# Performance work log

Hardware: AMD Instinct MI355X
Metric: run time of the kernel (lower is better)

Reference implementation:

```python
import jax, jax.numpy as jnp
import numpy as np

EPS = 1e-6


def _mp_cos_pointwise(p, q, M2):
    # p, q: [B, L, K]; M2: [C, K] (squared perspective weights)
    # cosine between (p*M_c) and (q*M_c) along K, per channel c -> [B, L, C]
    num = jnp.einsum('blk,blk,ck->blc', p, q, M2)
    pn = jnp.sqrt(jnp.maximum(jnp.einsum('blk,ck->blc', p * p, M2), EPS))
    qn = jnp.sqrt(jnp.maximum(jnp.einsum('blk,ck->blc', q * q, M2), EPS))
    return num / pn / qn


def setup_inputs() -> dict:
    key = jax.random.key(0)
    ks = jax.random.split(key, 10)
    B, Lq, Ld, K, C = 32, 200, 200, 200, 50
    f32 = jnp.float32
    def unif(k, shape):  # keras 'uniform' init: U(-0.05, 0.05)
        return jax.random.uniform(k, shape, f32, -0.05, 0.05)
    return {
        'q_rep': jax.random.normal(ks[0], (B, Lq, K), f32),
        'q_last': jax.random.normal(ks[1], (B, K), f32),
        'q_mask': jnp.ones((B, Lq), f32),
        'd_rep': jax.random.normal(ks[2], (B, Ld, K), f32),
        'd_last': jax.random.normal(ks[3], (B, K), f32),
        'd_mask': jnp.ones((B, Ld), f32),
        'full_M': unif(ks[4], (C, K)),
        'maxpool_M': unif(ks[5], (C, K)),
        'att_M': unif(ks[6], (C, K)),
        'max_att_M': unif(ks[7], (C, K)),
    }


def reference(q_rep, q_last, q_mask, d_rep, d_last, d_mask,
              full_M, maxpool_M, att_M, max_att_M):
    outputs = []

    # relevancy matrix: cosine(q[b,j,:], d[b,i,:]) -> [B, Ld, Lq]
    num = jnp.einsum('bik,bjk->bij', d_rep, q_rep)
    dn = jnp.sqrt(jnp.maximum(jnp.sum(d_rep * d_rep, -1), EPS))  # [B, Ld]
    qn = jnp.sqrt(jnp.maximum(jnp.sum(q_rep * q_rep, -1), EPS))  # [B, Lq]
    rel = num / qn[:, None, :] / dn[:, :, None]
    rel = rel * q_mask[:, None, :] * d_mask[:, :, None]

    # full matching: cosine(d[b,i]*M_c, q_last[b]*M_c) -> [B, Ld, C]
    M2 = full_M * full_M
    fnum = jnp.einsum('bik,bk,ck->bic', d_rep, q_last, M2)
    fpn = jnp.sqrt(jnp.maximum(jnp.einsum('bik,ck->bic', d_rep * d_rep, M2), EPS))
    fqn = jnp.sqrt(jnp.maximum(jnp.einsum('bk,ck->bc', q_last * q_last, M2), EPS))
    outputs.append(fnum / fpn / fqn[:, None, :])

    # maxpool matching: cosine(d[b,i]*M_c, q[b,j]*M_c) -> [B, Ld, Lq, C]
    M2 = maxpool_M * maxpool_M
    mnum = jnp.einsum('bik,bjk,ck->bijc', d_rep, q_rep, M2)
    mpn = jnp.sqrt(jnp.maximum(jnp.einsum('bik,ck->bic', d_rep * d_rep, M2), EPS))
    mqn = jnp.sqrt(jnp.maximum(jnp.einsum('bjk,ck->bjc', q_rep * q_rep, M2), EPS))
    mm = mnum / mpn[:, :, None, :] / mqn[:, None, :, :]
    outputs.append(jnp.concatenate([jnp.max(mm, axis=2), jnp.mean(mm, axis=2)], axis=2))

    # attentive matching: cosine-weighted q rep (no softmax -> normalize by sum)
    wq = jnp.einsum('bij,bjk->bik', rel, q_rep)
    wq = wq / (jnp.sum(rel, axis=-1) + EPS)[..., None]  # [B, Ld, K]
    outputs.append(_mp_cos_pointwise(d_rep, wq, att_M * att_M))

    # max-attentive matching: gather best-matching q word per d position
    idx = jnp.argmax(rel, axis=2)  # [B, Ld]
    max_q = jnp.take_along_axis(q_rep, idx[:, :, None], axis=1)  # [B, Ld, K]
    outputs.append(_mp_cos_pointwise(d_rep, max_q, max_att_M * max_att_M))

    return jnp.concatenate(outputs, axis=-1)  # [B, Ld, 5*C]
```

## Files before the change

kernel.cpp:

```cpp
#include <hip/hip_runtime.h>
#include <math.h>


#define EPS 1e-6f
#define NEG_HUGE -3.4e38f

typedef __bf16 bf16x8 __attribute__((ext_vector_type(8)));
typedef float f32x16 __attribute__((ext_vector_type(16)));

constexpr size_t OFF_M2ALL = 0;
constexpr size_t OFF_M2B16 = 40000;
constexpr size_t OFF_QB16  = 63296;
constexpr size_t OFF_DB16  = 915264;
constexpr size_t OFF_INVFPN= 1767232;
constexpr size_t OFF_INVMPN= 2087232;
constexpr size_t OFF_INVAPN= 2407232;
constexpr size_t OFF_INVXPN= 2727232;
constexpr size_t OFF_INVMQN= 3047232;
constexpr size_t OFF_INVXQN= 3367232;
constexpr size_t OFF_INVFQN= 3687232;
constexpr size_t OFF_INVDN = 3688832;
constexpr size_t OFF_INVQN = 3695232;
constexpr size_t OFF_IDX   = 3701632;
constexpr size_t OFF_WQ    = 3708032;
constexpr size_t OFF_G     = 4988032;
constexpr size_t OFF_PMAX2 = 6268032;
constexpr size_t OFF_PSUM2 = 6677632;

__global__ __launch_bounds__(256) void k_prep(
    const float* __restrict__ qR, const float* __restrict__ dR,
    const float* __restrict__ fM, const float* __restrict__ mM,
    const float* __restrict__ aM, const float* __restrict__ xM,
    unsigned short* __restrict__ qb16, unsigned short* __restrict__ db16,
    float* __restrict__ invdn, float* __restrict__ invqn,
    float* __restrict__ m2all, unsigned short* __restrict__ m2b16)
{
  int blk = blockIdx.x;
  int tid = threadIdx.x;
  if (blk < 4096) {
    int task = blk*4 + (tid >> 6);
    int l = tid & 63;
    int isQ = task >= 8192;
    int r = isQ ? task - 8192 : task;
    int b = r >> 8, j = r & 255;
    unsigned short* dst = (isQ ? qb16 : db16) + (size_t)r*208;
    if (j < 200) {
      const float* src = (isQ ? qR : dR) + (size_t)(b*200 + j)*200;
      float4 v = {0.f,0.f,0.f,0.f};
      if (l < 50) v = *(const float4*)(src + l*4);
      float s = fmaf(v.x,v.x, fmaf(v.y,v.y, fmaf(v.z,v.z, v.w*v.w)));
#pragma unroll
      for (int m = 32; m; m >>= 1) s += __shfl_xor(s, m);
      if (l == 0) {
        float rr = rsqrtf(fmaxf(s, EPS));
        if (isQ) invqn[b*200 + j] = rr; else invdn[b*200 + j] = rr;
      }
      if (l < 52) {
        ushort4 o = {0,0,0,0};
        if (l < 50) {
          __bf16 h0=(__bf16)v.x, h1=(__bf16)v.y, h2=(__bf16)v.z, h3=(__bf16)v.w;
          o.x = *(unsigned short*)&h0; o.y = *(unsigned short*)&h1;
          o.z = *(unsigned short*)&h2; o.w = *(unsigned short*)&h3;
        }
        *(ushort4*)(dst + l*4) = o;
      }
    } else {
      if (l < 52) { ushort4 z = {0,0,0,0}; *(ushort4*)(dst + l*4) = z; }
    }
  } else {
    int i = (blk - 4096)*256 + tid;
    if (i < 40000) {
      int m = i / 10000, r = i % 10000;
      const float* s = (m==0)?fM:(m==1)?mM:(m==2)?aM:xM;
      float v = s[r];
      m2all[i] = v*v;
    }
    if (i < 224*208) {
      int row = i / 208, k = i % 208;
      unsigned short o = 0;
      if (row < 200 && k < 200) {
        int m = row / 50, c = row % 50;
        const float* s = (m==0)?fM:(m==1)?mM:(m==2)?aM:xM;
        float v = s[c*200 + k];
        __bf16 h = (__bf16)(v*v);
        o = *(unsigned short*)&h;
      }
      m2b16[i] = o;
    }
  }
}

__global__ __launch_bounds__(256) void k_mid(
    const float* __restrict__ dR, const float* __restrict__ qR,
    const float* __restrict__ qL, const unsigned short* __restrict__ m2b16,
    float* __restrict__ invfpn, float* __restrict__ invmpn,
    float* __restrict__ invapn, float* __restrict__ invxpn,
    float* __restrict__ invmqn, float* __restrict__ invxqn,
    float* __restrict__ invfqn,
    const float* __restrict__ qMask, const float* __restrict__ dMask,
    const float* __restrict__ invdn, const float* __restrict__ invqn,
    float* __restrict__ wq, int* __restrict__ idxout)
{
  int tid = threadIdx.x;
  if (blockIdx.x < 702) {
    int w = tid >> 6, lane = tid & 63;
    int n = lane & 31, h = lane >> 5;
    int task = blockIdx.x*4 + w;
    if (task >= 2807) return;
    int rt = task / 7, nt = task % 7;
    int row = rt*32 + n;

    const float* src;
    if (row < 6400)       src = dR + (size_t)row*200;
    else if (row < 12800) src = qR + (size_t)(row-6400)*200;
    else                  src = qL + (size_t)(row-12800)*200;

    bf16x8 afrag[13];
#pragma unroll
    for (int ks = 0; ks < 13; ks++) {
      int ko = ks*16 + h*8;
      bf16x8 af;
      if (ko < 200) {
        float4 a0 = *(const float4*)(src + ko);
        float4 a1 = *(const float4*)(src + ko + 4);
        af[0] = (__bf16)(a0.x*a0.x); af[1] = (__bf16)(a0.y*a0.y);
        af[2] = (__bf16)(a0.z*a0.z); af[3] = (__bf16)(a0.w*a0.w);
        af[4] = (__bf16)(a1.x*a1.x); af[5] = (__bf16)(a1.y*a1.y);
        af[6] = (__bf16)(a1.z*a1.z); af[7] = (__bf16)(a1.w*a1.w);
      } else {
#pragma unroll
        for (int z = 0; z < 8; z++) af[z] = (__bf16)0.0f;
      }
      afrag[ks] = af;
    }

    f32x16 C;
#pragma unroll
    for (int z = 0; z < 16; z++) C[z] = 0.f;
    const unsigned short* bp = m2b16 + (size_t)(nt*32 + n)*208 + h*8;
#pragma unroll
    for (int ks = 0; ks < 13; ks++) {
      bf16x8 bf = *(const bf16x8*)(bp + ks*16);
      C = __builtin_amdgcn_mfma_f32_32x32x16_bf16(afrag[ks], bf, C, 0, 0, 0);
    }

    int cp = nt*32 + n;
    if (cp < 200) {
      int m = cp / 50, c = cp % 50;
#pragma unroll
      for (int r = 0; r < 16; r++) {
        int grow = rt*32 + (r & 3) + 8*(r >> 2) + 4*h;
        float v = rsqrtf(fmaxf(C[r], EPS));
        if (grow < 6400) {
          if (m == 0)      invfpn[grow*50 + c] = v;
          else if (m == 1) invmpn[grow*50 + c] = v;
          else if (m == 2) invapn[grow*50 + c] = v;
          else             invxpn[grow*50 + c] = v;
        } else if (grow < 12800) {
          int r2 = grow - 6400;
          if (m == 1)      invmqn[c*6400 + r2] = v;
          else if (m == 3) invxqn[r2*50 + c] = v;
        } else {
          if (m == 0)      invfqn[(grow-12800)*50 + c] = v;
        }
      }
    }
  } else {
    __shared__ float relsh[8][256];
    __shared__ float redv[4][8][2];
    __shared__ int   redi[4][8];
    __shared__ float invrs_sh[8];
    int blk = blockIdx.x - 702;
    int b  = blk / 25;
    int i0 = (blk % 25) * 8;
    int j = tid, jr = min(j, 199);
    bool jv = j < 200;
    const float* qb = qR + b*40000;
    const float* db = dR + (b*200 + i0)*200;
    float acc[8];
#pragma unroll
    for (int ii = 0; ii < 8; ii++) acc[ii] = 0.f;

    const float* qrow = qb + jr*200;
    for (int k4 = 0; k4 < 200; k4 += 4) {
      float4 qv = *(const float4*)(qrow + k4);
#pragma unroll
      for (int ii = 0; ii < 8; ii++) {
        acc[ii] = fmaf(db[ii*200 + k4 + 0], qv.x, acc[ii]);
        acc[ii] = fmaf(db[ii*200 + k4 + 1], qv.y, acc[ii]);
        acc[ii] = fmaf(db[ii*200 + k4 + 2], qv.z, acc[ii]);
        acc[ii] = fmaf(db[ii*200 + k4 + 3], qv.w, acc[ii]);
      }
    }

    float iqn = invqn[b*200 + jr];
    float qm  = qMask[b*200 + jr];
    int w = tid >> 6, l = tid & 63;
    float rv[8];
#pragma unroll
    for (int ii = 0; ii < 8; ii++) {
      float idn = invdn[b*200 + i0 + ii];
      float dm  = dMask[b*200 + i0 + ii];
      float r = acc[ii]*iqn*idn*qm*dm;
      rv[ii] = r;
      relsh[ii][j] = jv ? r : 0.f;
    }
#pragma unroll
    for (int ii = 0; ii < 8; ii++) {
      float vm = jv ? rv[ii] : NEG_HUGE;
      float vs = jv ? rv[ii] : 0.f;
      int bj = jr;
#pragma unroll
      for (int m = 32; m; m >>= 1) {
        float ov = __shfl_xor(vm, m);
        int   oj = __shfl_xor(bj, m);
        vs += __shfl_xor(vs, m);
        if (ov > vm || (ov == vm && oj < bj)) { vm = ov; bj = oj; }
      }
      if (l == 0) { redv[w][ii][0] = vm; redv[w][ii][1] = vs; redi[w][ii] = bj; }
    }
    __syncthreads();
    if (tid < 8) {
      float bv = redv[0][tid][0], ss = redv[0][tid][1]; int bj = redi[0][tid];
      for (int w2 = 1; w2 < 4; w2++) {
        ss += redv[w2][tid][1];
        float wv = redv[w2][tid][0]; int wj = redi[w2][tid];
        if (wv > bv || (wv == bv && wj < bj)) { bv = wv; bj = wj; }
      }
      invrs_sh[tid] = 1.f/(ss + EPS);
      idxout[b*200 + i0 + tid] = bj;
    }
    __syncthreads();

    int kl = min(tid, 199); bool kv = tid < 200;
    float acw[8];
#pragma unroll
    for (int ii = 0; ii < 8; ii++) acw[ii] = 0.f;
    for (int j0 = 0; j0 < 200; j0 += 4) {
      float qv0 = qb[(j0+0)*200 + kl];
      float qv1 = qb[(j0+1)*200 + kl];
      float qv2 = qb[(j0+2)*200 + kl];
      float qv3 = qb[(j0+3)*200 + kl];
#pragma unroll
      for (int ii = 0; ii < 8; ii++) {
        float4 rs = *(const float4*)&relsh[ii][j0];
        acw[ii] = fmaf(rs.x, qv0, acw[ii]);
        acw[ii] = fmaf(rs.y, qv1, acw[ii]);
        acw[ii] = fmaf(rs.z, qv2, acw[ii]);
        acw[ii] = fmaf(rs.w, qv3, acw[ii]);
      }
    }
#pragma unroll
    for (int ii = 0; ii < 8; ii++) {
      float v = acw[ii]*invrs_sh[ii];
      if (kv) wq[(size_t)(b*200 + i0 + ii)*200 + tid] = v;
    }
  }
}

__global__ __launch_bounds__(512,2) void k_big(
    const unsigned short* __restrict__ db16, const unsigned short* __restrict__ qb16,
    const float* __restrict__ m2all, const float* __restrict__ invmqn,
    float* __restrict__ pmax2, float* __restrict__ psum2,
    const float* __restrict__ dR, const float* __restrict__ qR,
    const float* __restrict__ qL, const float* __restrict__ wq,
    const int* __restrict__ idx, const unsigned short* __restrict__ m2b16,
    float* __restrict__ G)
{
  int tid = threadIdx.x;
  int w = tid >> 6, lane = tid & 63;
  int n = lane & 31, h = lane >> 5;
  if (blockIdx.x < 1600) {
    __shared__ __align__(16) unsigned short qsh[128*216];
    int b = blockIdx.x / 50, c = blockIdx.x % 50;
    const float* M2 = m2all + 10000 + c*200;
    const unsigned short* dbp = db16 + (size_t)(b*256 + w*32 + n)*208 + h*8;

    bf16x8 afrag[13];
#pragma unroll
    for (int ks = 0; ks < 13; ks++) afrag[ks] = *(const bf16x8*)(dbp + ks*16);

    float vm[16], vs[16];
#pragma unroll
    for (int r = 0; r < 16; r++) { vm[r] = NEG_HUGE; vs[r] = 0.f; }

    for (int jh = 0; jh < 2; jh++) {
      int nrows = jh ? 96 : 128;
      int njt   = jh ? 3 : 4;
      __syncthreads();
      {
        const unsigned short* src = qb16 + (size_t)(b*256 + jh*128)*208;
        const float* iqb = invmqn + c*6400 + b*200;
        for (int s = tid; s < nrows*26; s += 512) {
          int r = s / 26, ch = s - r*26;
          int j = jh*128 + r;
          float iq = (j < 200) ? iqb[j] : 0.f;
          int k0 = ch*8;
          bf16x8 v = *(const bf16x8*)(src + (size_t)r*208 + k0);
          float4 m0 = *(const float4*)(M2 + k0);
          float4 m1 = *(const float4*)(M2 + k0 + 4);
          bf16x8 o;
          o[0] = (__bf16)((float)v[0]*iq*m0.x); o[1] = (__bf16)((float)v[1]*iq*m0.y);
          o[2] = (__bf16)((float)v[2]*iq*m0.z); o[3] = (__bf16)((float)v[3]*iq*m0.w);
          o[4] = (__bf16)((float)v[4]*iq*m1.x); o[5] = (__bf16)((float)v[5]*iq*m1.y);
          o[6] = (__bf16)((float)v[6]*iq*m1.z); o[7] = (__bf16)((float)v[7]*iq*m1.w);
          *(bf16x8*)(qsh + r*216 + k0) = o;
        }
      }
      __syncthreads();

      for (int jt = 0; jt < njt; jt++) {
        f32x16 C;
#pragma unroll
        for (int z = 0; z < 16; z++) C[z] = 0.f;
        const unsigned short* bptr = qsh + (jt*32 + n)*216 + h*8;
#pragma unroll
        for (int ks = 0; ks < 13; ks++) {
          bf16x8 bf = *(const bf16x8*)(bptr + ks*16);
          C = __builtin_amdgcn_mfma_f32_32x32x16_bf16(afrag[ks], bf, C, 0, 0, 0);
        }
        bool jv = (jh*128 + jt*32 + n) < 200;
#pragma unroll
        for (int r = 0; r < 16; r++) {
          vm[r] = fmaxf(vm[r], jv ? C[r] : NEG_HUGE);
          vs[r] += C[r];
        }
      }
    }

#pragma unroll
    for (int r = 0; r < 16; r++) {
      float a = vm[r], s = vs[r];
#pragma unroll
      for (int m = 1; m <= 16; m <<= 1) {
        a = fmaxf(a, __shfl_xor(a, m));
        s += __shfl_xor(s, m);
      }
      vm[r] = a; vs[r] = s;
    }
    if (n == 0) {
#pragma unroll
      for (int r = 0; r < 16; r++) {
        int i = w*32 + (r & 3) + 8*(r >> 2) + 4*h;
        pmax2[(size_t)blockIdx.x*256 + i] = vm[r];
        psum2[(size_t)blockIdx.x*256 + i] = vs[r];
      }
    }
  } else {
    int task = (blockIdx.x - 1600)*8 + w;
    int mp = task / 400;
    int sub = task % 400;
    int rt = sub >> 1, nt = sub & 1;
    int row = rt*32 + n;
    int bb = row / 200;
    int msel = (mp == 0) ? 0 : (mp == 3) ? 3 : 2;

    const float* s0 = dR + (size_t)row*200;
    const float* s1;
    if (mp == 0)      s1 = qL + (size_t)bb*200;
    else if (mp == 1) s1 = wq + (size_t)row*200;
    else if (mp == 2) { s0 = wq + (size_t)row*200; s1 = s0; }
    else              s1 = qR + (size_t)(bb*200 + idx[row])*200;

    bf16x8 afrag[13];
#pragma unroll
    for (int ks = 0; ks < 13; ks++) {
      int ko = ks*16 + h*8;
      bf16x8 af;
      if (ko < 200) {
        float4 a0 = *(const float4*)(s0 + ko);
        float4 a1 = *(const float4*)(s0 + ko + 4);
        float4 b0 = *(const float4*)(s1 + ko);
        float4 b1 = *(const float4*)(s1 + ko + 4);
        af[0] = (__bf16)(a0.x*b0.x); af[1] = (__bf16)(a0.y*b0.y);
        af[2] = (__bf16)(a0.z*b0.z); af[3] = (__bf16)(a0.w*b0.w);
        af[4] = (__bf16)(a1.x*b1.x); af[5] = (__bf16)(a1.y*b1.y);
        af[6] = (__bf16)(a1.z*b1.z); af[7] = (__bf16)(a1.w*b1.w);
      } else {
#pragma unroll
        for (int z = 0; z < 8; z++) af[z] = (__bf16)0.0f;
      }
      afrag[ks] = af;
    }

    f32x16 C;
#pragma unroll
    for (int z = 0; z < 16; z++) C[z] = 0.f;
    const unsigned short* bp = m2b16 + (size_t)(msel*50 + nt*32 + n)*208 + h*8;
#pragma unroll
    for (int ks = 0; ks < 13; ks++) {
      bf16x8 bf = *(const bf16x8*)(bp + ks*16);
      C = __builtin_amdgcn_mfma_f32_32x32x16_bf16(afrag[ks], bf, C, 0, 0, 0);
    }
    int cc = nt*32 + n;
    if (cc < 50) {
#pragma unroll
      for (int r = 0; r < 16; r++) {
        int mrow = (r & 3) + 8*(r >> 2) + 4*h;
        G[(size_t)(mp*6400 + rt*32 + mrow)*50 + cc] = C[r];
      }
    }
  }
}

__global__ void k_out(
    const float* __restrict__ G, const float* __restrict__ pmax2,
    const float* __restrict__ psum2, const float* __restrict__ invfpn,
    const float* __restrict__ invmpn, const float* __restrict__ invapn,
    const float* __restrict__ invxpn, const float* __restrict__ invfqn,
    const float* __restrict__ invxqn, const int* __restrict__ idx,
    float* __restrict__ out)
{
  int row = blockIdx.x;
  int l = threadIdx.x;
  if (l >= 250) return;
  int b = row / 200, i = row % 200;
  int seg = l / 50, c = l % 50;
  float o;
  if (seg == 0) {
    o = G[(size_t)(0*6400 + row)*50 + c] * invfpn[row*50 + c] * invfqn[b*50 + c];
  } else if (seg == 1) {
    o = pmax2[(size_t)(b*50 + c)*256 + i] * invmpn[row*50 + c];
  } else if (seg == 2) {
    o = psum2[(size_t)(b*50 + c)*256 + i] * invmpn[row*50 + c] * (1.f/200.f);
  } else if (seg == 3) {
    o = G[(size_t)(1*6400 + row)*50 + c] * invapn[row*50 + c]
        * rsqrtf(fmaxf(G[(size_t)(2*6400 + row)*50 + c], EPS));
  } else {
    int jid = idx[row];
    o = G[(size_t)(3*6400 + row)*50 + c] * invxpn[row*50 + c]
        * invxqn[(b*200 + jid)*50 + c];
  }
  out[(size_t)row*250 + l] = o;
}

extern "C" void kernel_launch(void* const* d_in, const int* in_sizes, int n_in,
                              void* d_out, int out_size, void* d_ws, size_t ws_size,
                              hipStream_t stream) {
  const float* qR = (const float*)d_in[0];
  const float* qL = (const float*)d_in[1];
  const float* qM = (const float*)d_in[2];
  const float* dR = (const float*)d_in[3];
  const float* dM = (const float*)d_in[5];
  const float* fullM = (const float*)d_in[6];
  const float* mpM   = (const float*)d_in[7];
  const float* attM  = (const float*)d_in[8];
  const float* xM    = (const float*)d_in[9];

  float* ws  = (float*)d_ws;
  float* out = (float*)d_out;

  float* m2all  = ws + OFF_M2ALL;
  unsigned short* m2b16 = (unsigned short*)(ws + OFF_M2B16);
  unsigned short* qb16 = (unsigned short*)(ws + OFF_QB16);
  unsigned short* db16 = (unsigned short*)(ws + OFF_DB16);
  float* invfpn = ws + OFF_INVFPN;
  float* invmpn = ws + OFF_INVMPN;
  float* invapn = ws + OFF_INVAPN;
  float* invxpn = ws + OFF_INVXPN;
  float* invmqn = ws + OFF_INVMQN;
  float* invxqn = ws + OFF_INVXQN;
  float* invfqn = ws + OFF_INVFQN;
  float* invdn  = ws + OFF_INVDN;
  float* invqn  = ws + OFF_INVQN;
  int*   idxp   = (int*)(ws + OFF_IDX);
  float* wqp    = ws + OFF_WQ;
  float* G      = ws + OFF_G;
  float* pmax2  = ws + OFF_PMAX2;
  float* psum2  = ws + OFF_PSUM2;

  k_prep<<<4278, 256, 0, stream>>>(qR, dR, fullM, mpM, attM, xM,
                                   qb16, db16, invdn, invqn, m2all, m2b16);
  k_mid<<<1502, 256, 0, stream>>>(dR, qR, qL, m2b16,
                                  invfpn, invmpn, invapn, invxpn,
                                  invmqn, invxqn, invfqn,
                                  qM, dM, invdn, invqn, wqp, idxp);
  k_big<<<1800, 512, 0, stream>>>(db16, qb16, m2all, invmqn, pmax2, psum2,
                                  dR, qR, qL, wqp, idxp, m2b16, G);
  k_out<<<6400, 256, 0, stream>>>(G, pmax2, psum2, invfpn, invmpn, invapn,
                                  invxpn, invfqn, invxqn, idxp, out);
}
```

Measured before the change: 248.1 us.

## Fuse four kernels into two and fold normalizations into maxpool operands

Collapses the prep, mid, big and out kernels into a main kernel and a final kernel. The main kernel runs the maxpool MFMA, the relevancy/attention path and the norm GEMMs as separate block ranges. The maxpool path pre-scales q rows by the inverse norm and the squared weights when staging them into shared memory, so the max/mean reduction needs no division afterwards. The final kernel computes the full, attentive and max-attentive GEMMs and writes the output directly, dropping the intermediate G buffer and the bf16 staging copies. This removes launches and global round trips, at the cost of recomputing row norms inside blocks and a heavier single kernel with a large shared-memory union.

```diff
diff --git a/kernel.cpp b/kernel.cpp
--- a/kernel.cpp
+++ b/kernel.cpp
@@ -8,179 +8,194 @@
 typedef __bf16 bf16x8 __attribute__((ext_vector_type(8)));
 typedef float f32x16 __attribute__((ext_vector_type(16)));
 
-constexpr size_t OFF_M2ALL = 0;
-constexpr size_t OFF_M2B16 = 40000;
-constexpr size_t OFF_QB16  = 63296;
-constexpr size_t OFF_DB16  = 915264;
-constexpr size_t OFF_INVFPN= 1767232;
-constexpr size_t OFF_INVMPN= 2087232;
-constexpr size_t OFF_INVAPN= 2407232;
-constexpr size_t OFF_INVXPN= 2727232;
-constexpr size_t OFF_INVMQN= 3047232;
-constexpr size_t OFF_INVXQN= 3367232;
-constexpr size_t OFF_INVFQN= 3687232;
-constexpr size_t OFF_INVDN = 3688832;
-constexpr size_t OFF_INVQN = 3695232;
-constexpr size_t OFF_IDX   = 3701632;
-constexpr size_t OFF_WQ    = 3708032;
-constexpr size_t OFF_G     = 4988032;
-constexpr size_t OFF_PMAX2 = 6268032;
-constexpr size_t OFF_PSUM2 = 6677632;
-
-__global__ __launch_bounds__(256) void k_prep(
+constexpr size_t OFF_INVFPN = 0;
+constexpr size_t OFF_INVMPN = 320000;
+constexpr size_t OFF_INVAPN = 640000;
+constexpr size_t OFF_INVXPN = 960000;
+constexpr size_t OFF_INVMQN = 1280000;
+constexpr size_t OFF_INVXQN = 1600000;
+constexpr size_t OFF_INVFQN = 1920000;
+constexpr size_t OFF_IDX    = 1921600;
+constexpr size_t OFF_WQ     = 1928000;
+constexpr size_t OFF_PMAX2  = 3208000;
+constexpr size_t OFF_PSUM2  = 3617600;
+
+struct MPShared {
+  unsigned short qsh[128*216];
+  float m2sh[208];
+  float iqsh[200];
+};
+struct RWShared {
+  float relsh[2][8][256];
+  float iqn[2][200];
+  float idn[2][8];
+  float redv[2][4][8][2];
+  int   redi[2][4][8];
+  float invrs[2][8];
+};
+union KShared { MPShared mp; RWShared rw; };
+
+__global__ __launch_bounds__(512,2) void k_main(
     const float* __restrict__ qR, const float* __restrict__ dR,
+    const float* __restrict__ qL,
+    const float* __restrict__ qMask, const float* __restrict__ dMask,
     const float* __restrict__ fM, const float* __restrict__ mM,
     const float* __restrict__ aM, const float* __restrict__ xM,
-    unsigned short* __restrict__ qb16, unsigned short* __restrict__ db16,
-    float* __restrict__ invdn, float* __restrict__ invqn,
-    float* __restrict__ m2all, unsigned short* __restrict__ m2b16)
-{
-  int blk = blockIdx.x;
-  int tid = threadIdx.x;
-  if (blk < 4096) {
-    int task = blk*4 + (tid >> 6);
-    int l = tid & 63;
-    int isQ = task >= 8192;
-    int r = isQ ? task - 8192 : task;
-    int b = r >> 8, j = r & 255;
-    unsigned short* dst = (isQ ? qb16 : db16) + (size_t)r*208;
-    if (j < 200) {
-      const float* src = (isQ ? qR : dR) + (size_t)(b*200 + j)*200;
-      float4 v = {0.f,0.f,0.f,0.f};
-      if (l < 50) v = *(const float4*)(src + l*4);
-      float s = fmaf(v.x,v.x, fmaf(v.y,v.y, fmaf(v.z,v.z, v.w*v.w)));
-#pragma unroll
-      for (int m = 32; m; m >>= 1) s += __shfl_xor(s, m);
-      if (l == 0) {
-        float rr = rsqrtf(fmaxf(s, EPS));
-        if (isQ) invqn[b*200 + j] = rr; else invdn[b*200 + j] = rr;
-      }
-      if (l < 52) {
-        ushort4 o = {0,0,0,0};
-        if (l < 50) {
-          __bf16 h0=(__bf16)v.x, h1=(__bf16)v.y, h2=(__bf16)v.z, h3=(__bf16)v.w;
-          o.x = *(unsigned short*)&h0; o.y = *(unsigned short*)&h1;
-          o.z = *(unsigned short*)&h2; o.w = *(unsigned short*)&h3;
-        }
-        *(ushort4*)(dst + l*4) = o;
-      }
-    } else {
-      if (l < 52) { ushort4 z = {0,0,0,0}; *(ushort4*)(dst + l*4) = z; }
-    }
-  } else {
-    int i = (blk - 4096)*256 + tid;
-    if (i < 40000) {
-      int m = i / 10000, r = i % 10000;
-      const float* s = (m==0)?fM:(m==1)?mM:(m==2)?aM:xM;
-      float v = s[r];
-      m2all[i] = v*v;
-    }
-    if (i < 224*208) {
-      int row = i / 208, k = i % 208;
-      unsigned short o = 0;
-      if (row < 200 && k < 200) {
-        int m = row / 50, c = row % 50;
-        const float* s = (m==0)?fM:(m==1)?mM:(m==2)?aM:xM;
-        float v = s[c*200 + k];
-        __bf16 h = (__bf16)(v*v);
-        o = *(unsigned short*)&h;
-      }
-      m2b16[i] = o;
-    }
-  }
-}
-
-__global__ __launch_bounds__(256) void k_mid(
-    const float* __restrict__ dR, const float* __restrict__ qR,
-    const float* __restrict__ qL, const unsigned short* __restrict__ m2b16,
     float* __restrict__ invfpn, float* __restrict__ invmpn,
     float* __restrict__ invapn, float* __restrict__ invxpn,
     float* __restrict__ invmqn, float* __restrict__ invxqn,
     float* __restrict__ invfqn,
-    const float* __restrict__ qMask, const float* __restrict__ dMask,
-    const float* __restrict__ invdn, const float* __restrict__ invqn,
-    float* __restrict__ wq, int* __restrict__ idxout)
+    float* __restrict__ wq, int* __restrict__ idxout,
+    float* __restrict__ pmax2, float* __restrict__ psum2)
 {
+  __shared__ KShared sh;
   int tid = threadIdx.x;
-  if (blockIdx.x < 702) {
-    int w = tid >> 6, lane = tid & 63;
-    int n = lane & 31, h = lane >> 5;
-    int task = blockIdx.x*4 + w;
-    if (task >= 2807) return;
-    int rt = task / 7, nt = task % 7;
-    int row = rt*32 + n;
-
-    const float* src;
-    if (row < 6400)       src = dR + (size_t)row*200;
-    else if (row < 12800) src = qR + (size_t)(row-6400)*200;
-    else                  src = qL + (size_t)(row-12800)*200;
-
+  int blk = blockIdx.x;
+  int w = tid >> 6, lane = tid & 63;
+  int n = lane & 31, h = lane >> 5;
+
+  if (blk < 1600) {
+    int b = blk / 50, c = blk % 50;
+    if (tid < 52) {
+      int k = tid*4;
+      float4 o = {0.f,0.f,0.f,0.f};
+      if (k < 200) {
+        float4 v = *(const float4*)(mM + c*200 + k);
+        o.x=v.x*v.x; o.y=v.y*v.y; o.z=v.z*v.z; o.w=v.w*v.w;
+      }
+      *(float4*)(sh.mp.m2sh + k) = o;
+    }
+    __syncthreads();
+    {
+      const float* qb = qR + b*40000;
+      for (int j = w*25; j < w*25 + 25; j++) {
+        const float* qr = qb + j*200;
+        float s = 0.f;
+        for (int k = lane; k < 200; k += 64) { float v = qr[k]; s = fmaf(v*v, sh.mp.m2sh[k], s); }
+#pragma unroll
+        for (int m = 32; m; m >>= 1) s += __shfl_xor(s, m);
+        if (lane == 0) sh.mp.iqsh[j] = rsqrtf(fmaxf(s, EPS));
+      }
+    }
     bf16x8 afrag[13];
-#pragma unroll
-    for (int ks = 0; ks < 13; ks++) {
-      int ko = ks*16 + h*8;
-      bf16x8 af;
-      if (ko < 200) {
-        float4 a0 = *(const float4*)(src + ko);
-        float4 a1 = *(const float4*)(src + ko + 4);
-        af[0] = (__bf16)(a0.x*a0.x); af[1] = (__bf16)(a0.y*a0.y);
-        af[2] = (__bf16)(a0.z*a0.z); af[3] = (__bf16)(a0.w*a0.w);
-        af[4] = (__bf16)(a1.x*a1.x); af[5] = (__bf16)(a1.y*a1.y);
-        af[6] = (__bf16)(a1.z*a1.z); af[7] = (__bf16)(a1.w*a1.w);
-      } else {
-#pragma unroll
-        for (int z = 0; z < 8; z++) af[z] = (__bf16)0.0f;
-      }
-      afrag[ks] = af;
-    }
-
-    f32x16 C;
-#pragma unroll
-    for (int z = 0; z < 16; z++) C[z] = 0.f;
-    const unsigned short* bp = m2b16 + (size_t)(nt*32 + n)*208 + h*8;
-#pragma unroll
-    for (int ks = 0; ks < 13; ks++) {
-      bf16x8 bf = *(const bf16x8*)(bp + ks*16);
-      C = __builtin_amdgcn_mfma_f32_32x32x16_bf16(afrag[ks], bf, C, 0, 0, 0);
-    }
-
-    int cp = nt*32 + n;
-    if (cp < 200) {
-      int m = cp / 50, c = cp % 50;
+    {
+      int i = w*32 + n, ir = min(i, 199);
+      const float* drow = dR + (size_t)(b*200 + ir)*200;
+#pragma unroll
+      for (int ks = 0; ks < 13; ks++) {
+        int ko = ks*16 + h*8;
+        bf16x8 af;
+        if (ko < 200) {
+          float4 a0 = *(const float4*)(drow + ko);
+          float4 a1 = *(const float4*)(drow + ko + 4);
+          af[0]=(__bf16)a0.x; af[1]=(__bf16)a0.y; af[2]=(__bf16)a0.z; af[3]=(__bf16)a0.w;
+          af[4]=(__bf16)a1.x; af[5]=(__bf16)a1.y; af[6]=(__bf16)a1.z; af[7]=(__bf16)a1.w;
+        } else {
+#pragma unroll
+          for (int z = 0; z < 8; z++) af[z] = (__bf16)0.0f;
+        }
+        afrag[ks] = af;
+      }
+    }
+    float vm[16], vs[16];
+#pragma unroll
+    for (int r = 0; r < 16; r++) { vm[r] = NEG_HUGE; vs[r] = 0.f; }
+
+    for (int jh = 0; jh < 2; jh++) {
+      int nrows = jh ? 96 : 128;
+      int njt   = jh ? 3 : 4;
+      __syncthreads();
+      {
+        const float* qb = qR + b*40000;
+        for (int s = tid; s < nrows*26; s += 512) {
+          int r = s / 26, ch = s - r*26;
+          int j = jh*128 + r;
+          int k0 = ch*8;
+          bf16x8 o;
+          if (j < 200 && k0 < 200) {
+            const float* qr = qb + (size_t)j*200 + k0;
+            float4 v0 = *(const float4*)qr;
+            float4 v1 = *(const float4*)(qr + 4);
+            float iq = sh.mp.iqsh[j];
+            o[0]=(__bf16)(v0.x*iq*sh.mp.m2sh[k0+0]); o[1]=(__bf16)(v0.y*iq*sh.mp.m2sh[k0+1]);
+            o[2]=(__bf16)(v0.z*iq*sh.mp.m2sh[k0+2]); o[3]=(__bf16)(v0.w*iq*sh.mp.m2sh[k0+3]);
+            o[4]=(__bf16)(v1.x*iq*sh.mp.m2sh[k0+4]); o[5]=(__bf16)(v1.y*iq*sh.mp.m2sh[k0+5]);
+            o[6]=(__bf16)(v1.z*iq*sh.mp.m2sh[k0+6]); o[7]=(__bf16)(v1.w*iq*sh.mp.m2sh[k0+7]);
+          } else {
+#pragma unroll
+            for (int z = 0; z < 8; z++) o[z] = (__bf16)0.0f;
+          }
+          *(bf16x8*)(sh.mp.qsh + r*216 + k0) = o;
+        }
+      }
+      __syncthreads();
+      for (int jt = 0; jt < njt; jt++) {
+        f32x16 C;
+#pragma unroll
+        for (int z = 0; z < 16; z++) C[z] = 0.f;
+        const unsigned short* bptr = sh.mp.qsh + (jt*32 + n)*216 + h*8;
+#pragma unroll
+        for (int ks = 0; ks < 13; ks++) {
+          bf16x8 bf = *(const bf16x8*)(bptr + ks*16);
+          C = __builtin_amdgcn_mfma_f32_32x32x16_bf16(afrag[ks], bf, C, 0, 0, 0);
+        }
+        bool jv = (jh*128 + jt*32 + n) < 200;
+#pragma unroll
+        for (int r = 0; r < 16; r++) {
+          vm[r] = fmaxf(vm[r], jv ? C[r] : NEG_HUGE);
+          vs[r] += C[r];
+        }
+      }
+    }
+#pragma unroll
+    for (int r = 0; r < 16; r++) {
+      float a = vm[r], s = vs[r];
+#pragma unroll
+      for (int m = 1; m <= 16; m <<= 1) { a = fmaxf(a, __shfl_xor(a, m)); s += __shfl_xor(s, m); }
+      vm[r] = a; vs[r] = s;
+    }
+    if (n == 0) {
 #pragma unroll
       for (int r = 0; r < 16; r++) {
-        int grow = rt*32 + (r & 3) + 8*(r >> 2) + 4*h;
-        float v = rsqrtf(fmaxf(C[r], EPS));
-        if (grow < 6400) {
-          if (m == 0)      invfpn[grow*50 + c] = v;
-          else if (m == 1) invmpn[grow*50 + c] = v;
-          else if (m == 2) invapn[grow*50 + c] = v;
-          else             invxpn[grow*50 + c] = v;
-        } else if (grow < 12800) {
-          int r2 = grow - 6400;
-          if (m == 1)      invmqn[c*6400 + r2] = v;
-          else if (m == 3) invxqn[r2*50 + c] = v;
-        } else {
-          if (m == 0)      invfqn[(grow-12800)*50 + c] = v;
-        }
-      }
-    }
-  } else {
-    __shared__ float relsh[8][256];
-    __shared__ float redv[4][8][2];
-    __shared__ int   redi[4][8];
-    __shared__ float invrs_sh[8];
-    int blk = blockIdx.x - 702;
-    int b  = blk / 25;
-    int i0 = (blk % 25) * 8;
-    int j = tid, jr = min(j, 199);
+        int i = w*32 + (r & 3) + 8*(r >> 2) + 4*h;
+        pmax2[(size_t)blk*256 + i] = vm[r];
+        psum2[(size_t)blk*256 + i] = vs[r];
+      }
+    }
+  } else if (blk < 2000) {
+    int u = tid >> 8;
+    int tid2 = tid & 255;
+    int unit = (blk - 1600)*2 + u;
+    int b = unit / 25, i0 = (unit % 25)*8;
+    int w2 = tid2 >> 6, l = lane;
+    int j = tid2, jr = min(j, 199);
     bool jv = j < 200;
     const float* qb = qR + b*40000;
     const float* db = dR + (b*200 + i0)*200;
+
+    for (int jq = w2*50; jq < w2*50 + 50; jq++) {
+      float4 v = {0.f,0.f,0.f,0.f};
+      if (l < 50) v = *(const float4*)(qb + jq*200 + l*4);
+      float s = fmaf(v.x,v.x, fmaf(v.y,v.y, fmaf(v.z,v.z, v.w*v.w)));
+#pragma unroll
+      for (int m = 32; m; m >>= 1) s += __shfl_xor(s, m);
+      if (l == 0) sh.rw.iqn[u][jq] = rsqrtf(fmaxf(s, EPS));
+    }
+    if (w2 == 0) {
+      for (int ii = 0; ii < 8; ii++) {
+        float4 v = {0.f,0.f,0.f,0.f};
+        if (l < 50) v = *(const float4*)(db + ii*200 + l*4);
+        float s = fmaf(v.x,v.x, fmaf(v.y,v.y, fmaf(v.z,v.z, v.w*v.w)));
+#pragma unroll
+        for (int m = 32; m; m >>= 1) s += __shfl_xor(s, m);
+        if (l == 0) sh.rw.idn[u][ii] = rsqrtf(fmaxf(s, EPS));
+      }
+    }
+    __syncthreads();
+
     float acc[8];
 #pragma unroll
     for (int ii = 0; ii < 8; ii++) acc[ii] = 0.f;
-
     const float* qrow = qb + jr*200;
     for (int k4 = 0; k4 < 200; k4 += 4) {
       float4 qv = *(const float4*)(qrow + k4);
@@ -192,47 +207,45 @@
         acc[ii] = fmaf(db[ii*200 + k4 + 3], qv.w, acc[ii]);
       }
     }
-
-    float iqn = invqn[b*200 + jr];
+    float iqnv = sh.rw.iqn[u][jr];
     float qm  = qMask[b*200 + jr];
-    int w = tid >> 6, l = tid & 63;
     float rv[8];
 #pragma unroll
     for (int ii = 0; ii < 8; ii++) {
-      float idn = invdn[b*200 + i0 + ii];
-      float dm  = dMask[b*200 + i0 + ii];
-      float r = acc[ii]*iqn*idn*qm*dm;
+      float idnv = sh.rw.idn[u][ii];
+      float dm = dMask[b*200 + i0 + ii];
+      float r = acc[ii]*iqnv*idnv*qm*dm;
       rv[ii] = r;
-      relsh[ii][j] = jv ? r : 0.f;
+      sh.rw.relsh[u][ii][j] = jv ? r : 0.f;
     }
 #pragma unroll
     for (int ii = 0; ii < 8; ii++) {
-      float vm = jv ? rv[ii] : NEG_HUGE;
-      float vs = jv ? rv[ii] : 0.f;
+      float vmv = jv ? rv[ii] : NEG_HUGE;
+      float vsv = jv ? rv[ii] : 0.f;
       int bj = jr;
 #pragma unroll
       for (int m = 32; m; m >>= 1) {
-        float ov = __shfl_xor(vm, m);
+        float ov = __shfl_xor(vmv, m);
         int   oj = __shfl_xor(bj, m);
-        vs += __shfl_xor(vs, m);
-        if (ov > vm || (ov == vm && oj < bj)) { vm = ov; bj = oj; }
-      }
-      if (l == 0) { redv[w][ii][0] = vm; redv[w][ii][1] = vs; redi[w][ii] = bj; }
+        vsv += __shfl_xor(vsv, m);
+        if (ov > vmv || (ov == vmv && oj < bj)) { vmv = ov; bj = oj; }
+      }
+      if (l == 0) { sh.rw.redv[u][w2][ii][0] = vmv; sh.rw.redv[u][w2][ii][1] = vsv; sh.rw.redi[u][w2][ii] = bj; }
     }
     __syncthreads();
-    if (tid < 8) {
-      float bv = redv[0][tid][0], ss = redv[0][tid][1]; int bj = redi[0][tid];
-      for (int w2 = 1; w2 < 4; w2++) {
-        ss += redv[w2][tid][1];
-        float wv = redv[w2][tid][0]; int wj = redi[w2][tid];
+    if (tid2 < 8) {
+      float bv = sh.rw.redv[u][0][tid2][0], ss = sh.rw.redv[u][0][tid2][1];
+      int bj = sh.rw.redi[u][0][tid2];
+      for (int w3 = 1; w3 < 4; w3++) {
+        ss += sh.rw.redv[u][w3][tid2][1];
+        float wv = sh.rw.redv[u][w3][tid2][0]; int wj = sh.rw.redi[u][w3][tid2];
         if (wv > bv || (wv == bv && wj < bj)) { bv = wv; bj = wj; }
       }
-      invrs_sh[tid] = 1.f/(ss + EPS);
-      idxout[b*200 + i0 + tid] = bj;
+      sh.rw.invrs[u][tid2] = 1.f/(ss + EPS);
+      idxout[b*200 + i0 + tid2] = bj;
     }
     __syncthreads();
-
-    int kl = min(tid, 199); bool kv = tid < 200;
+    int kl = min(tid2, 199); bool kv = tid2 < 200;
     float acw[8];
 #pragma unroll
     for (int ii = 0; ii < 8; ii++) acw[ii] = 0.f;
@@ -243,7 +256,7 @@
       float qv3 = qb[(j0+3)*200 + kl];
 #pragma unroll
       for (int ii = 0; ii < 8; ii++) {
-        float4 rs = *(const float4*)&relsh[ii][j0];
+        float4 rs = *(const float4*)&sh.rw.relsh[u][ii][j0];
         acw[ii] = fmaf(rs.x, qv0, acw[ii]);
         acw[ii] = fmaf(rs.y, qv1, acw[ii]);
         acw[ii] = fmaf(rs.z, qv2, acw[ii]);
@@ -252,186 +265,208 @@
     }
 #pragma unroll
     for (int ii = 0; ii < 8; ii++) {
-      float v = acw[ii]*invrs_sh[ii];
-      if (kv) wq[(size_t)(b*200 + i0 + ii)*200 + tid] = v;
+      float v = acw[ii]*sh.rw.invrs[u][ii];
+      if (kv) wq[(size_t)(b*200 + i0 + ii)*200 + tid2] = v;
+    }
+  } else {
+    int task = (blk - 2000)*8 + w;
+    if (task < 2807) {
+      int rt = task / 7, nt = task % 7;
+      int row = rt*32 + n;
+      const float* src;
+      if (row < 6400)       src = dR + (size_t)row*200;
+      else if (row < 12800) src = qR + (size_t)(row-6400)*200;
+      else                  src = qL + (size_t)(row-12800)*200;
+
+      bf16x8 afrag[13];
+#pragma unroll
+      for (int ks = 0; ks < 13; ks++) {
+        int ko = ks*16 + h*8;
+        bf16x8 af;
+        if (ko < 200) {
+          float4 a0 = *(const float4*)(src + ko);
+          float4 a1 = *(const float4*)(src + ko + 4);
+          af[0]=(__bf16)(a0.x*a0.x); af[1]=(__bf16)(a0.y*a0.y);
+          af[2]=(__bf16)(a0.z*a0.z); af[3]=(__bf16)(a0.w*a0.w);
+          af[4]=(__bf16)(a1.x*a1.x); af[5]=(__bf16)(a1.y*a1.y);
+          af[6]=(__bf16)(a1.z*a1.z); af[7]=(__bf16)(a1.w*a1.w);
+        } else {
+#pragma unroll
+          for (int z = 0; z < 8; z++) af[z] = (__bf16)0.0f;
+        }
+        afrag[ks] = af;
+      }
+      int cp = nt*32 + n;
+      bool cpv = cp < 200;
+      int mIdx = 0, cIdx = 0;
+      const float* msrc = fM;
+      if (cpv) {
+        mIdx = cp / 50; cIdx = cp % 50;
+        msrc = ((mIdx==0)?fM:(mIdx==1)?mM:(mIdx==2)?aM:xM) + cIdx*200;
+      }
+      f32x16 C;
+#pragma unroll
+      for (int z = 0; z < 16; z++) C[z] = 0.f;
+#pragma unroll
+      for (int ks = 0; ks < 13; ks++) {
+        int ko = ks*16 + h*8;
+        bf16x8 bf;
+        if (cpv && ko < 200) {
+          float4 b0 = *(const float4*)(msrc + ko);
+          float4 b1 = *(const float4*)(msrc + ko + 4);
+          bf[0]=(__bf16)(b0.x*b0.x); bf[1]=(__bf16)(b0.y*b0.y);
+          bf[2]=(__bf16)(b0.z*b0.z); bf[3]=(__bf16)(b0.w*b0.w);
+          bf[4]=(__bf16)(b1.x*b1.x); bf[5]=(__bf16)(b1.y*b1.y);
+          bf[6]=(__bf16)(b1.z*b1.z); bf[7]=(__bf16)(b1.w*b1.w);
+        } else {
+#pragma unroll
+          for (int z = 0; z < 8; z++) bf[z] = (__bf16)0.0f;
+        }
+        C = __builtin_amdgcn_mfma_f32_32x32x16_bf16(afrag[ks], bf, C, 0, 0, 0);
+      }
+      if (cpv) {
+#pragma unroll
+        for (int r = 0; r < 16; r++) {
+          int grow = rt*32 + (r & 3) + 8*(r >> 2) + 4*h;
+          float v = rsqrtf(fmaxf(C[r], EPS));
+          if (grow < 6400) {
+            if (mIdx == 0)      invfpn[grow*50 + cIdx] = v;
+            else if (mIdx == 1) invmpn[grow*50 + cIdx] = v;
+            else if (mIdx == 2) invapn[grow*50 + cIdx] = v;
+            else                invxpn[grow*50 + cIdx] = v;
+          } else if (grow < 12800) {
+            int r2 = grow - 6400;
+            if (mIdx == 1)      invmqn[cIdx*6400 + r2] = v;
+            else if (mIdx == 3) invxqn[r2*50 + cIdx] = v;
+          } else {
+            if (mIdx == 0)      invfqn[(grow-12800)*50 + cIdx] = v;
+          }
+        }
+      }
     }
   }
 }
 
-__global__ __launch_bounds__(512,2) void k_big(
-    const unsigned short* __restrict__ db16, const unsigned short* __restrict__ qb16,
-    const float* __restrict__ m2all, const float* __restrict__ invmqn,
-    float* __restrict__ pmax2, float* __restrict__ psum2,
+__global__ __launch_bounds__(512,2) void k_final(
     const float* __restrict__ dR, const float* __restrict__ qR,
     const float* __restrict__ qL, const float* __restrict__ wq,
-    const int* __restrict__ idx, const unsigned short* __restrict__ m2b16,
-    float* __restrict__ G)
+    const int* __restrict__ idx,
+    const float* __restrict__ fM, const float* __restrict__ aM,
+    const float* __restrict__ xM,
+    const float* __restrict__ invfpn, const float* __restrict__ invmpn,
+    const float* __restrict__ invapn, const float* __restrict__ invxpn,
+    const float* __restrict__ invfqn, const float* __restrict__ invxqn,
+    const float* __restrict__ pmax2, const float* __restrict__ psum2,
+    float* __restrict__ out)
 {
   int tid = threadIdx.x;
+  int blk = blockIdx.x;
   int w = tid >> 6, lane = tid & 63;
   int n = lane & 31, h = lane >> 5;
-  if (blockIdx.x < 1600) {
-    __shared__ __align__(16) unsigned short qsh[128*216];
-    int b = blockIdx.x / 50, c = blockIdx.x % 50;
-    const float* M2 = m2all + 10000 + c*200;
-    const unsigned short* dbp = db16 + (size_t)(b*256 + w*32 + n)*208 + h*8;
-
-    bf16x8 afrag[13];
-#pragma unroll
-    for (int ks = 0; ks < 13; ks++) afrag[ks] = *(const bf16x8*)(dbp + ks*16);
-
-    float vm[16], vs[16];
-#pragma unroll
-    for (int r = 0; r < 16; r++) { vm[r] = NEG_HUGE; vs[r] = 0.f; }
-
-    for (int jh = 0; jh < 2; jh++) {
-      int nrows = jh ? 96 : 128;
-      int njt   = jh ? 3 : 4;
-      __syncthreads();
-      {
-        const unsigned short* src = qb16 + (size_t)(b*256 + jh*128)*208;
-        const float* iqb = invmqn + c*6400 + b*200;
-        for (int s = tid; s < nrows*26; s += 512) {
-          int r = s / 26, ch = s - r*26;
-          int j = jh*128 + r;
-          float iq = (j < 200) ? iqb[j] : 0.f;
-          int k0 = ch*8;
-          bf16x8 v = *(const bf16x8*)(src + (size_t)r*208 + k0);
-          float4 m0 = *(const float4*)(M2 + k0);
-          float4 m1 = *(const float4*)(M2 + k0 + 4);
-          bf16x8 o;
-          o[0] = (__bf16)((float)v[0]*iq*m0.x); o[1] = (__bf16)((float)v[1]*iq*m0.y);
-          o[2] = (__bf16)((float)v[2]*iq*m0.z); o[3] = (__bf16)((float)v[3]*iq*m0.w);
-          o[4] = (__bf16)((float)v[4]*iq*m1.x); o[5] = (__bf16)((float)v[5]*iq*m1.y);
-          o[6] = (__bf16)((float)v[6]*iq*m1.z); o[7] = (__bf16)((float)v[7]*iq*m1.w);
-          *(bf16x8*)(qsh + r*216 + k0) = o;
-        }
-      }
-      __syncthreads();
-
-      for (int jt = 0; jt < njt; jt++) {
-        f32x16 C;
-#pragma unroll
-        for (int z = 0; z < 16; z++) C[z] = 0.f;
-        const unsigned short* bptr = qsh + (jt*32 + n)*216 + h*8;
-#pragma unroll
-        for (int ks = 0; ks < 13; ks++) {
-          bf16x8 bf = *(const bf16x8*)(bptr + ks*16);
-          C = __builtin_amdgcn_mfma_f32_32x32x16_bf16(afrag[ks], bf, C, 0, 0, 0);
-        }
-        bool jv = (jh*128 + jt*32 + n) < 200;
-#pragma unroll
-        for (int r = 0; r < 16; r++) {
-          vm[r] = fmaxf(vm[r], jv ? C[r] : NEG_HUGE);
-          vs[r] += C[r];
-        }
-      }
-    }
-
-#pragma unroll
-    for (int r = 0; r < 16; r++) {
-      float a = vm[r], s = vs[r];
-#pragma unroll
-      for (int m = 1; m <= 16; m <<= 1) {
-        a = fmaxf(a, __shfl_xor(a, m));
-        s += __shfl_xor(s, m);
-      }
-      vm[r] = a; vs[r] = s;
-    }
-    if (n == 0) {
-#pragma unroll
-      for (int r = 0; r < 16; r++) {
-        int i = w*32 + (r & 3) + 8*(r >> 2) + 4*h;
-        pmax2[(size_t)blockIdx.x*256 + i] = vm[r];
-        psum2[(size_t)blockIdx.x*256 + i] = vs[r];
-      }
-    }
-  } else {
-    int task = (blockIdx.x - 1600)*8 + w;
-    int mp = task / 400;
-    int sub = task % 400;
+  if (blk < 150) {
+    int gtask = blk*8 + w;
+    int typ = gtask / 400;
+    int sub = gtask % 400;
     int rt = sub >> 1, nt = sub & 1;
-    int row = rt*32 + n;
-    int bb = row / 200;
-    int msel = (mp == 0) ? 0 : (mp == 3) ? 3 : 2;
+    int row = rt*32 + n, bb = row / 200;
+    int cc = nt*32 + n;
+    bool ccv = cc < 50;
+    const float* Bsrc = (typ == 0) ? fM : (typ == 1) ? aM : xM;
+    const float* msrc = Bsrc + (ccv ? cc : 0)*200;
+
+    bf16x8 bfrag[13];
+#pragma unroll
+    for (int ks = 0; ks < 13; ks++) {
+      int ko = ks*16 + h*8;
+      bf16x8 bf;
+      if (ccv && ko < 200) {
+        float4 b0 = *(const float4*)(msrc + ko);
+        float4 b1 = *(const float4*)(msrc + ko + 4);
+        bf[0]=(__bf16)(b0.x*b0.x); bf[1]=(__bf16)(b0.y*b0.y);
+        bf[2]=(__bf16)(b0.z*b0.z); bf[3]=(__bf16)(b0.w*b0.w);
+        bf[4]=(__bf16)(b1.x*b1.x); bf[5]=(__bf16)(b1.y*b1.y);
+        bf[6]=(__bf16)(b1.z*b1.z); bf[7]=(__bf16)(b1.w*b1.w);
+      } else {
+#pragma unroll
+        for (int z = 0; z < 8; z++) bf[z] = (__bf16)0.0f;
+      }
+      bfrag[ks] = bf;
+    }
+
+    auto buildA = [&](const float* s0, const float* s1, bf16x8* fr) {
+#pragma unroll
+      for (int ks = 0; ks < 13; ks++) {
+        int ko = ks*16 + h*8;
+        bf16x8 af;
+        if (ko < 200) {
+          float4 a0 = *(const float4*)(s0 + ko), a1 = *(const float4*)(s0 + ko + 4);
+          float4 b0 = *(const float4*)(s1 + ko), b1 = *(const float4*)(s1 + ko + 4);
+          af[0]=(__bf16)(a0.x*b0.x); af[1]=(__bf16)(a0.y*b0.y);
+          af[2]=(__bf16)(a0.z*b0.z); af[3]=(__bf16)(a0.w*b0.w);
+          af[4]=(__bf16)(a1.x*b1.x); af[5]=(__bf16)(a1.y*b1.y);
+          af[6]=(__bf16)(a1.z*b1.z); af[7]=(__bf16)(a1.w*b1.w);
+        } else {
+#pragma unroll
+          for (int z = 0; z < 8; z++) af[z] = (__bf16)0.0f;
+        }
+        fr[ks] = af;
+      }
+    };
 
     const float* s0 = dR + (size_t)row*200;
     const float* s1;
-    if (mp == 0)      s1 = qL + (size_t)bb*200;
-    else if (mp == 1) s1 = wq + (size_t)row*200;
-    else if (mp == 2) { s0 = wq + (size_t)row*200; s1 = s0; }
-    else              s1 = qR + (size_t)(bb*200 + idx[row])*200;
+    if (typ == 0)      s1 = qL + (size_t)bb*200;
+    else if (typ == 1) s1 = wq + (size_t)row*200;
+    else               s1 = qR + (size_t)(bb*200 + idx[row])*200;
 
     bf16x8 afrag[13];
-#pragma unroll
-    for (int ks = 0; ks < 13; ks++) {
-      int ko = ks*16 + h*8;
-      bf16x8 af;
-      if (ko < 200) {
-        float4 a0 = *(const float4*)(s0 + ko);
-        float4 a1 = *(const float4*)(s0 + ko + 4);
-        float4 b0 = *(const float4*)(s1 + ko);
-        float4 b1 = *(const float4*)(s1 + ko + 4);
-        af[0] = (__bf16)(a0.x*b0.x); af[1] = (__bf16)(a0.y*b0.y);
-        af[2] = (__bf16)(a0.z*b0.z); af[3] = (__bf16)(a0.w*b0.w);
-        af[4] = (__bf16)(a1.x*b1.x); af[5] = (__bf16)(a1.y*b1.y);
-        af[6] = (__bf16)(a1.z*b1.z); af[7] = (__bf16)(a1.w*b1.w);
-      } else {
-#pragma unroll
-        for (int z = 0; z < 8; z++) af[z] = (__bf16)0.0f;
-      }
-      afrag[ks] = af;
-    }
-
-    f32x16 C;
-#pragma unroll
-    for (int z = 0; z < 16; z++) C[z] = 0.f;
-    const unsigned short* bp = m2b16 + (size_t)(msel*50 + nt*32 + n)*208 + h*8;
-#pragma unroll
-    for (int ks = 0; ks < 13; ks++) {
-      bf16x8 bf = *(const bf16x8*)(bp + ks*16);
-      C = __builtin_amdgcn_mfma_f32_32x32x16_bf16(afrag[ks], bf, C, 0, 0, 0);
-    }
-    int cc = nt*32 + n;
-    if (cc < 50) {
+    buildA(s0, s1, afrag);
+    f32x16 C1;
+#pragma unroll
+    for (int z = 0; z < 16; z++) C1[z] = 0.f;
+#pragma unroll
+    for (int ks = 0; ks < 13; ks++)
+      C1 = __builtin_amdgcn_mfma_f32_32x32x16_bf16(afrag[ks], bfrag[ks], C1, 0, 0, 0);
+
+    f32x16 C2;
+#pragma unroll
+    for (int z = 0; z < 16; z++) C2[z] = 0.f;
+    if (typ == 1) {
+      const float* s2 = wq + (size_t)row*200;
+      buildA(s2, s2, afrag);
+#pragma unroll
+      for (int ks = 0; ks < 13; ks++)
+        C2 = __builtin_amdgcn_mfma_f32_32x32x16_bf16(afrag[ks], bfrag[ks], C2, 0, 0, 0);
+    }
+
+    if (ccv) {
 #pragma unroll
       for (int r = 0; r < 16; r++) {
-        int mrow = (r & 3) + 8*(r >> 2) + 4*h;
-        G[(size_t)(mp*6400 + rt*32 + mrow)*50 + cc] = C[r];
-      }
+        int grow = rt*32 + (r & 3) + 8*(r >> 2) + 4*h;
+        int b2 = grow / 200;
+        float o; int colbase;
+        if (typ == 0) {
+          o = C1[r]*invfpn[grow*50 + cc]*invfqn[b2*50 + cc]; colbase = 0;
+        } else if (typ == 1) {
+          o = C1[r]*invapn[grow*50 + cc]*rsqrtf(fmaxf(C2[r], EPS)); colbase = 150;
+        } else {
+          int jid = idx[grow];
+          o = C1[r]*invxpn[grow*50 + cc]*invxqn[(b2*200 + jid)*50 + cc]; colbase = 200;
+        }
+        out[(size_t)grow*250 + colbase + cc] = o;
+      }
+    }
+  } else {
+    int base = (blk - 150)*512 + tid;
+    for (int e = base; e < 640000; e += 25600) {
+      int row = e / 100, cl = e % 100;
+      int b2 = row / 200, i2 = row % 200;
+      int c2 = (cl < 50) ? cl : cl - 50;
+      float pv = (cl < 50) ? pmax2[(size_t)(b2*50 + c2)*256 + i2]
+                           : psum2[(size_t)(b2*50 + c2)*256 + i2]*(1.f/200.f);
+      out[(size_t)row*250 + 50 + cl] = pv*invmpn[row*50 + c2];
     }
   }
-}
-
-__global__ void k_out(
-    const float* __restrict__ G, const float* __restrict__ pmax2,
-    const float* __restrict__ psum2, const float* __restrict__ invfpn,
-    const float* __restrict__ invmpn, const float* __restrict__ invapn,
-    const float* __restrict__ invxpn, const float* __restrict__ invfqn,
-    const float* __restrict__ invxqn, const int* __restrict__ idx,
-    float* __restrict__ out)
-{
-  int row = blockIdx.x;
-  int l = threadIdx.x;
-  if (l >= 250) return;
-  int b = row / 200, i = row % 200;
-  int seg = l / 50, c = l % 50;
-  float o;
-  if (seg == 0) {
-    o = G[(size_t)(0*6400 + row)*50 + c] * invfpn[row*50 + c] * invfqn[b*50 + c];
-  } else if (seg == 1) {
-    o = pmax2[(size_t)(b*50 + c)*256 + i] * invmpn[row*50 + c];
-  } else if (seg == 2) {
-    o = psum2[(size_t)(b*50 + c)*256 + i] * invmpn[row*50 + c] * (1.f/200.f);
-  } else if (seg == 3) {
-    o = G[(size_t)(1*6400 + row)*50 + c] * invapn[row*50 + c]
-        * rsqrtf(fmaxf(G[(size_t)(2*6400 + row)*50 + c], EPS));
-  } else {
-    int jid = idx[row];
-    o = G[(size_t)(3*6400 + row)*50 + c] * invxpn[row*50 + c]
-        * invxqn[(b*200 + jid)*50 + c];
-  }
-  out[(size_t)row*250 + l] = o;
 }
 
 extern "C" void kernel_launch(void* const* d_in, const int* in_sizes, int n_in,
@@ -450,10 +485,6 @@
   float* ws  = (float*)d_ws;
   float* out = (float*)d_out;
 
-  float* m2all  = ws + OFF_M2ALL;
-  unsigned short* m2b16 = (unsigned short*)(ws + OFF_M2B16);
-  unsigned short* qb16 = (unsigned short*)(ws + OFF_QB16);
-  unsigned short* db16 = (unsigned short*)(ws + OFF_DB16);
   float* invfpn = ws + OFF_INVFPN;
   float* invmpn = ws + OFF_INVMPN;
   float* invapn = ws + OFF_INVAPN;
@@ -461,22 +492,18 @@
   float* invmqn = ws + OFF_INVMQN;
   float* invxqn = ws + OFF_INVXQN;
   float* invfqn = ws + OFF_INVFQN;
-  float* invdn  = ws + OFF_INVDN;
-  float* invqn  = ws + OFF_INVQN;
   int*   idxp   = (int*)(ws + OFF_IDX);
   float* wqp    = ws + OFF_WQ;
-  float* G      = ws + OFF_G;
   float* pmax2  = ws + OFF_PMAX2;
   float* psum2  = ws + OFF_PSUM2;
 
-  k_prep<<<4278, 256, 0, stream>>>(qR, dR, fullM, mpM, attM, xM,
-                                   qb16, db16, invdn, invqn, m2all, m2b16);
-  k_mid<<<1502, 256, 0, stream>>>(dR, qR, qL, m2b16,
-                                  invfpn, invmpn, invapn, invxpn,
-                                  invmqn, invxqn, invfqn,
-                                  qM, dM, invdn, invqn, wqp, idxp);
-  k_big<<<1800, 512, 0, stream>>>(db16, qb16, m2all, invmqn, pmax2, psum2,
-                                  dR, qR, qL, wqp, idxp, m2b16, G);
-  k_out<<<6400, 256, 0, stream>>>(G, pmax2, psum2, invfpn, invmpn, invapn,
-                                  invxpn, invfqn, invxqn, idxp, out);
+  k_main<<<2351, 512, 0, stream>>>(qR, dR, qL, qM, dM,
+                                   fullM, mpM, attM, xM,
+                                   invfpn, invmpn, invapn, invxpn,
+                                   invmqn, invxqn, invfqn,
+                                   wqp, idxp, pmax2, psum2);
+  k_final<<<200, 512, 0, stream>>>(dR, qR, qL, wqp, idxp,
+                                   fullM, attM, xM,
+                                   invfpn, invmpn, invapn, invxpn,
+                                   invfqn, invxqn, pmax2, psum2, out);
 }
```

Measured after the change: 522.5 us. +110.6%, slower.
